# Kernel optimization log

Measured on AMD Instinct MI355X. Metric: run time of the kernel, lower is better.

The kernel has to match this reference:

```python
import jax, jax.numpy as jnp
import numpy as np

B, N, D, H = 2, 2048, 128, 128  # batch, n_nodes, node_dim, hidden_dim
HQ = H // 4
EPS_DIST = 1e-8
EPS_LN = 1e-5


def setup_inputs() -> dict:
    key = jax.random.key(0)
    ks = jax.random.split(key, 12)
    s = 0.02
    return {
        "h": jax.random.normal(ks[0], (B, N, D), jnp.float32),
        "coords": jax.random.uniform(ks[1], (B, N, 2), jnp.float32),
        "Wq": jax.random.normal(ks[2], (D, H), jnp.float32) * s,
        "bq": jnp.zeros((H,), jnp.float32),
        "Wk": jax.random.normal(ks[3], (D, H), jnp.float32) * s,
        "bk": jnp.zeros((H,), jnp.float32),
        "Wv": jax.random.normal(ks[4], (D, H), jnp.float32) * s,
        "bv": jnp.zeros((H,), jnp.float32),
        "Wd1": jax.random.normal(ks[5], (1, HQ), jnp.float32) * s,
        "bd1": jnp.zeros((HQ,), jnp.float32),
        "Wd2": jax.random.normal(ks[6], (HQ, 1), jnp.float32) * s,
        "bd2": jnp.zeros((1,), jnp.float32),
        "Wo": jax.random.normal(ks[7], (H, D), jnp.float32) * s,
        "bo": jnp.zeros((D,), jnp.float32),
        "gamma": jnp.ones((D,), jnp.float32),
        "beta": jnp.zeros((D,), jnp.float32),
    }


def reference(h, coords, Wq, bq, Wk, bk, Wv, bv, Wd1, bd1, Wd2, bd2, Wo, bo, gamma, beta):
    q = h @ Wq + bq                      # (B, N, H)
    k = h @ Wk + bk
    v = h @ Wv + bv
    scores = jnp.einsum('bnh,bmh->bnm', q, k) / jnp.sqrt(jnp.float32(H))  # (B,N,N)
    # pairwise Euclidean distances
    diff = coords[:, :, None, :] - coords[:, None, :, :]                  # (B,N,N,2)
    dist = jnp.sqrt(jnp.sum(diff * diff, axis=-1, keepdims=True) + EPS_DIST)  # (B,N,N,1)
    hmid = jax.nn.silu(dist @ Wd1 + bd1)                                  # (B,N,N,HQ)
    dist_bias = (hmid @ Wd2 + bd2)[..., 0]                                # (B,N,N)
    attn = jax.nn.softmax(scores + dist_bias, axis=-1)
    out = jnp.einsum('bnm,bmh->bnh', attn, v)                             # (B,N,H)
    out = jax.nn.silu(out @ Wo + bo)                                      # (B,N,D)
    res = h + out
    mu = jnp.mean(res, axis=-1, keepdims=True)
    var = jnp.mean((res - mu) ** 2, axis=-1, keepdims=True)
    return (res - mu) / jnp.sqrt(var + EPS_LN) * gamma + beta
```

## Files before the change

### kernel.cpp

```cpp
#include <hip/hip_runtime.h>
#include <hip/hip_bf16.h>

#define B_ 2
#define N_ 2048
#define D_ 128
#define H_ 128
#define HQ_ 32
#define ROWS_ (B_*N_)
#define KS_ 16
#define KPP_ (N_/KS_)
#define DMAX_ 1.4143f
#define SCALE_ 0.08838834764831845f

typedef __bf16 bf16x8 __attribute__((ext_vector_type(8)));
typedef float  f32x4  __attribute__((ext_vector_type(4)));
typedef unsigned short ushort8 __attribute__((ext_vector_type(8)));

#define Q_OFF    0
#define K_OFF    (ROWS_*H_*2)
#define V_OFF    (2*ROWS_*H_*2)
#define L_OFF    (3*ROWS_*H_*2)
#define OP_OFF   (L_OFF + ROWS_*KS_*4)

__global__ __launch_bounds__(384) void qkv_kernel(
    const float* __restrict__ h,
    const float* __restrict__ Wq, const float* __restrict__ bq,
    const float* __restrict__ Wk, const float* __restrict__ bk,
    const float* __restrict__ Wv, const float* __restrict__ bv,
    __bf16* __restrict__ qb, __bf16* __restrict__ kb, __bf16* __restrict__ vb)
{
    __shared__ __align__(16) float hs[8][128];
    const int t = threadIdx.x;
    const int row0 = blockIdx.x * 8;
    for (int idx = t; idx < 1024; idx += 384) hs[idx >> 7][idx & 127] = h[row0 * 128 + idx];
    __syncthreads();

    const int which = t >> 7;
    const int c = t & 127;
    const float* W    = which == 0 ? Wq : (which == 1 ? Wk : Wv);
    const float* bias = which == 0 ? bq : (which == 1 ? bk : bv);
    __bf16* outp      = which == 0 ? qb : (which == 1 ? kb : vb);
    const float scale = which == 0 ? SCALE_ : 1.f;

    float acc[8];
    #pragma unroll
    for (int r = 0; r < 8; ++r) acc[r] = 0.f;

    #pragma unroll 8
    for (int d = 0; d < 128; ++d) {
        float w = W[d * 128 + c];
        #pragma unroll
        for (int r = 0; r < 8; ++r) acc[r] = fmaf(hs[r][d], w, acc[r]);
    }
    const float bvv = bias[c];
    #pragma unroll
    for (int r = 0; r < 8; ++r)
        outp[(size_t)(row0 + r) * 128 + c] = (__bf16)((acc[r] + bvv) * scale);
}

__global__ __launch_bounds__(256, 4) void attn_kernel(
    const __bf16* __restrict__ qb, const __bf16* __restrict__ kb, const __bf16* __restrict__ vb,
    const float* __restrict__ coords,
    const float* __restrict__ Wd1, const float* __restrict__ bd1,
    const float* __restrict__ Wd2, const float* __restrict__ bd2,
    __bf16* __restrict__ Opb, float* __restrict__ Larr)
{
    __shared__ __align__(16) unsigned int Vsu[2][128][20];
    __shared__ __align__(16) __bf16 Pl[4][16][40];

    const int t    = threadIdx.x;
    const int wid  = t >> 6;
    const int lane = t & 63;
    const int l16  = lane & 15;
    const int g    = lane >> 4;
    const int qbase = blockIdx.x * 64 + wid * 16;
    const int p     = blockIdx.y;
    const int b     = qbase >> 11;

    float c0, c1, c2, c3, c4;
    {
        const int j = lane & 31;
        const float w1 = Wd1[j], b1 = bd1[j];
        const float w2h = Wd2[j] * 0.5f;
        float gv[5];
        #pragma unroll
        for (int i = 0; i < 5; ++i) {
            float d = (DMAX_ * 0.25f) * (float)i;
            float x = fmaf(d, w1, b1);
            gv[i] = (x / (1.f + __expf(-x))) * w2h;
        }
        #pragma unroll
        for (int i = 0; i < 5; ++i)
            #pragma unroll
            for (int off = 1; off < 64; off <<= 1) gv[i] += __shfl_xor(gv[i], off);
        const float bd2v = bd2[0];
        float g0 = gv[0] + bd2v, g1 = gv[1] + bd2v, g2 = gv[2] + bd2v,
              g3 = gv[3] + bd2v, g4 = gv[4] + bd2v;
        c0 = g0;
        c1 = -2.0833333333f*g0 + 4.f*g1 - 3.f*g2 + 1.3333333333f*g3 - 0.25f*g4;
        c2 =  1.4583333333f*g0 - 4.3333333333f*g1 + 4.75f*g2 - 2.3333333333f*g3 + 0.4583333333f*g4;
        c3 = -0.4166666667f*g0 + 1.5f*g1 - 2.f*g2 + 1.1666666667f*g3 - 0.25f*g4;
        c4 =  0.0416666667f*g0 - 0.1666666667f*g1 + 0.25f*g2 - 0.1666666667f*g3 + 0.0416666667f*g4;
    }

    bf16x8 qf[4];
    const __bf16* qrow = qb + (size_t)(qbase + l16) * H_;
    #pragma unroll
    for (int kk = 0; kk < 4; ++kk) qf[kk] = *(const bf16x8*)(qrow + kk * 32 + g * 8);

    float cx[4], cy[4];
    #pragma unroll
    for (int i = 0; i < 4; ++i) {
        int qr = qbase + g * 4 + i;
        cx[i] = coords[qr * 2]; cy[i] = coords[qr * 2 + 1];
    }

    float l_i[4] = {0.f, 0.f, 0.f, 0.f};
    f32x4 O[8];
    #pragma unroll
    for (int c = 0; c < 8; ++c) O[c] = (f32x4){0.f, 0.f, 0.f, 0.f};

    const int kp = t & 15, co = t >> 4;
    const int kgbase = (b << 11) + p * KPP_;
    const int NT = KPP_ / 32;

    {
        const __bf16* sp = vb + (size_t)(kgbase + 2 * kp) * H_ + co * 8;
        bf16x8 va = *(const bf16x8*)sp;
        bf16x8 vb2 = *(const bf16x8*)(sp + H_);
        ushort8 ua = __builtin_bit_cast(ushort8, va);
        ushort8 ub = __builtin_bit_cast(ushort8, vb2);
        #pragma unroll
        for (int j = 0; j < 8; ++j)
            Vsu[0][co * 8 + j][kp] = (unsigned)ua[j] | ((unsigned)ub[j] << 16);
    }

    for (int kt = 0; kt < NT; ++kt) {
        __syncthreads();

        bf16x8 nva, nvb;
        if (kt + 1 < NT) {
            const __bf16* sp = vb + (size_t)(kgbase + (kt + 1) * 32 + 2 * kp) * H_ + co * 8;
            nva = *(const bf16x8*)sp;
            nvb = *(const bf16x8*)(sp + H_);
        }

        const int kg = kgbase + kt * 32;
        #pragma unroll
        for (int mt = 0; mt < 2; ++mt) {
            f32x4 acc = (f32x4){0.f, 0.f, 0.f, 0.f};
            const __bf16* krow = kb + (size_t)(kg + mt * 16 + l16) * H_;
            #pragma unroll
            for (int kk = 0; kk < 4; ++kk) {
                bf16x8 kf = *(const bf16x8*)(krow + kk * 32 + g * 8);
                acc = __builtin_amdgcn_mfma_f32_16x16x32_bf16(qf[kk], kf, acc, 0, 0, 0);
            }
            float2 kc = *(const float2*)&coords[(kg + mt * 16 + l16) * 2];
            #pragma unroll
            for (int i = 0; i < 4; ++i) {
                float dx = cx[i] - kc.x, dy = cy[i] - kc.y;
                float dist = sqrtf(fmaf(dx, dx, fmaf(dy, dy, 1e-8f)));
                float s4 = dist * (4.0f / DMAX_);
                float bias = fmaf(fmaf(fmaf(fmaf(c4, s4, c3), s4, c2), s4, c1), s4, c0);
                float sc = fminf(acc[i] + bias, 60.f);
                float pe = __expf(sc);
                l_i[i] += pe;
                Pl[wid][g * 4 + i][mt * 16 + l16] = (__bf16)pe;
            }
        }

        if (kt + 1 < NT) {
            ushort8 ua = __builtin_bit_cast(ushort8, nva);
            ushort8 ub = __builtin_bit_cast(ushort8, nvb);
            #pragma unroll
            for (int j = 0; j < 8; ++j)
                Vsu[(kt + 1) & 1][co * 8 + j][kp] = (unsigned)ua[j] | ((unsigned)ub[j] << 16);
        }

        bf16x8 pf = *(const bf16x8*)&Pl[wid][l16][g * 8];
        #pragma unroll
        for (int c = 0; c < 8; ++c) {
            bf16x8 vf = *(const bf16x8*)&Vsu[kt & 1][c * 16 + l16][g * 4];
            O[c] = __builtin_amdgcn_mfma_f32_16x16x32_bf16(pf, vf, O[c], 0, 0, 0);
        }
    }

    #pragma unroll
    for (int c = 0; c < 8; ++c)
        #pragma unroll
        for (int i = 0; i < 4; ++i)
            Opb[((size_t)p * ROWS_ + qbase + g * 4 + i) * H_ + c * 16 + l16] = (__bf16)O[c][i];

    #pragma unroll
    for (int i = 0; i < 4; ++i) {
        float lv = l_i[i];
        lv += __shfl_xor(lv, 1); lv += __shfl_xor(lv, 2);
        lv += __shfl_xor(lv, 4); lv += __shfl_xor(lv, 8);
        if (l16 == 0) Larr[(qbase + g * 4 + i) * KS_ + p] = lv;
    }
}

__global__ __launch_bounds__(128) void final_kernel(
    const __bf16* __restrict__ Opb, const float* __restrict__ Larr,
    const float* __restrict__ h, const float* __restrict__ Wo, const float* __restrict__ bo,
    const float* __restrict__ gamma, const float* __restrict__ beta, float* __restrict__ out)
{
    __shared__ __align__(16) float as_[4][128];
    __shared__ float redS[2][4], redQ[2][4];
    const int t = threadIdx.x;
    const int row0 = blockIdx.x * 4;

    #pragma unroll
    for (int r = 0; r < 4; ++r) {
        int row = row0 + r;
        float acc = 0.f, lsum = 0.f;
        #pragma unroll
        for (int p = 0; p < KS_; ++p) {
            acc  += (float)Opb[((size_t)p * ROWS_ + row) * H_ + t];
            lsum += Larr[row * KS_ + p];
        }
        as_[r][t] = acc / lsum;
    }
    __syncthreads();

    float acc4[4] = {0.f, 0.f, 0.f, 0.f};
    #pragma unroll 4
    for (int d4 = 0; d4 < 32; ++d4) {
        float w0 = Wo[(d4 * 4 + 0) * 128 + t];
        float w1 = Wo[(d4 * 4 + 1) * 128 + t];
        float w2 = Wo[(d4 * 4 + 2) * 128 + t];
        float w3 = Wo[(d4 * 4 + 3) * 128 + t];
        #pragma unroll
        for (int r = 0; r < 4; ++r) {
            f32x4 a_ = *(const f32x4*)&as_[r][d4 * 4];
            acc4[r] = fmaf(a_[0], w0, acc4[r]);
            acc4[r] = fmaf(a_[1], w1, acc4[r]);
            acc4[r] = fmaf(a_[2], w2, acc4[r]);
            acc4[r] = fmaf(a_[3], w3, acc4[r]);
        }
    }

    const float bov = bo[t], gv = gamma[t], bvv = beta[t];
    const int wh = t >> 6;
    float res[4];
    #pragma unroll
    for (int r = 0; r < 4; ++r) {
        float x = acc4[r] + bov;
        float sl = x / (1.f + __expf(-x));
        res[r] = h[(size_t)(row0 + r) * 128 + t] + sl;
    }

    #pragma unroll
    for (int r = 0; r < 4; ++r) {
        float s1 = res[r], s2 = res[r] * res[r];
        #pragma unroll
        for (int off = 32; off >= 1; off >>= 1) {
            s1 += __shfl_xor(s1, off);
            s2 += __shfl_xor(s2, off);
        }
        if ((t & 63) == 0) { redS[wh][r] = s1; redQ[wh][r] = s2; }
    }
    __syncthreads();
    #pragma unroll
    for (int r = 0; r < 4; ++r) {
        float sum = redS[0][r] + redS[1][r];
        float sq  = redQ[0][r] + redQ[1][r];
        float mu  = sum * (1.f / 128.f);
        float var = sq * (1.f / 128.f) - mu * mu;
        out[(size_t)(row0 + r) * 128 + t] = (res[r] - mu) * rsqrtf(var + 1e-5f) * gv + bvv;
    }
}

extern "C" void kernel_launch(void* const* d_in, const int* in_sizes, int n_in,
                              void* d_out, int out_size, void* d_ws, size_t ws_size,
                              hipStream_t stream)
{
    const float* h      = (const float*)d_in[0];
    const float* coords = (const float*)d_in[1];
    const float* Wq = (const float*)d_in[2];  const float* bq = (const float*)d_in[3];
    const float* Wk = (const float*)d_in[4];  const float* bk = (const float*)d_in[5];
    const float* Wv = (const float*)d_in[6];  const float* bv = (const float*)d_in[7];
    const float* Wd1 = (const float*)d_in[8]; const float* bd1 = (const float*)d_in[9];
    const float* Wd2 = (const float*)d_in[10];const float* bd2 = (const float*)d_in[11];
    const float* Wo = (const float*)d_in[12]; const float* bo = (const float*)d_in[13];
    const float* gamma = (const float*)d_in[14]; const float* beta = (const float*)d_in[15];

    char* ws = (char*)d_ws;
    __bf16* qb = (__bf16*)(ws + Q_OFF);
    __bf16* kb = (__bf16*)(ws + K_OFF);
    __bf16* vb = (__bf16*)(ws + V_OFF);
    float* Larr  = (float*)(ws + L_OFF);
    __bf16* Opb  = (__bf16*)(ws + OP_OFF);

    qkv_kernel<<<ROWS_ / 8, 384, 0, stream>>>(h, Wq, bq, Wk, bk, Wv, bv, qb, kb, vb);
    attn_kernel<<<dim3(ROWS_ / 64, KS_), 256, 0, stream>>>(qb, kb, vb, coords,
                                                           Wd1, bd1, Wd2, bd2, Opb, Larr);
    final_kernel<<<ROWS_ / 4, 128, 0, stream>>>(Opb, Larr, h, Wo, bo, gamma, beta, (float*)d_out);
}
```

Measured before the change: 59.12 us.

## Use exp2 with folded log2e, pack partial outputs, enlarge qkv and final tiles

```diff
diff --git a/kernel.cpp b/kernel.cpp
--- a/kernel.cpp
+++ b/kernel.cpp
@@ -11,10 +11,22 @@
 #define KPP_ (N_/KS_)
 #define DMAX_ 1.4143f
 #define SCALE_ 0.08838834764831845f
+#define LOG2E_ 1.4426950408889634f
 
 typedef __bf16 bf16x8 __attribute__((ext_vector_type(8)));
 typedef float  f32x4  __attribute__((ext_vector_type(4)));
 typedef unsigned short ushort8 __attribute__((ext_vector_type(8)));
+
+#if __has_builtin(__builtin_amdgcn_exp2f)
+#define EXP2F_ __builtin_amdgcn_exp2f
+#else
+#define EXP2F_ exp2f
+#endif
+#if __has_builtin(__builtin_amdgcn_sqrtf)
+#define SQRTF_ __builtin_amdgcn_sqrtf
+#else
+#define SQRTF_ sqrtf
+#endif
 
 #define Q_OFF    0
 #define K_OFF    (ROWS_*H_*2)
@@ -29,10 +41,10 @@
     const float* __restrict__ Wv, const float* __restrict__ bv,
     __bf16* __restrict__ qb, __bf16* __restrict__ kb, __bf16* __restrict__ vb)
 {
-    __shared__ __align__(16) float hs[8][128];
+    __shared__ __align__(16) float hs[16][128];
     const int t = threadIdx.x;
-    const int row0 = blockIdx.x * 8;
-    for (int idx = t; idx < 1024; idx += 384) hs[idx >> 7][idx & 127] = h[row0 * 128 + idx];
+    const int row0 = blockIdx.x * 16;
+    for (int idx = t; idx < 2048; idx += 384) hs[idx >> 7][idx & 127] = h[row0 * 128 + idx];
     __syncthreads();
 
     const int which = t >> 7;
@@ -40,21 +52,21 @@
     const float* W    = which == 0 ? Wq : (which == 1 ? Wk : Wv);
     const float* bias = which == 0 ? bq : (which == 1 ? bk : bv);
     __bf16* outp      = which == 0 ? qb : (which == 1 ? kb : vb);
-    const float scale = which == 0 ? SCALE_ : 1.f;
-
-    float acc[8];
-    #pragma unroll
-    for (int r = 0; r < 8; ++r) acc[r] = 0.f;
+    const float scale = which == 0 ? (SCALE_ * LOG2E_) : 1.f;
+
+    float acc[16];
+    #pragma unroll
+    for (int r = 0; r < 16; ++r) acc[r] = 0.f;
 
     #pragma unroll 8
     for (int d = 0; d < 128; ++d) {
         float w = W[d * 128 + c];
         #pragma unroll
-        for (int r = 0; r < 8; ++r) acc[r] = fmaf(hs[r][d], w, acc[r]);
+        for (int r = 0; r < 16; ++r) acc[r] = fmaf(hs[r][d], w, acc[r]);
     }
     const float bvv = bias[c];
     #pragma unroll
-    for (int r = 0; r < 8; ++r)
+    for (int r = 0; r < 16; ++r)
         outp[(size_t)(row0 + r) * 128 + c] = (__bf16)((acc[r] + bvv) * scale);
 }
 
@@ -63,7 +75,7 @@
     const float* __restrict__ coords,
     const float* __restrict__ Wd1, const float* __restrict__ bd1,
     const float* __restrict__ Wd2, const float* __restrict__ bd2,
-    __bf16* __restrict__ Opb, float* __restrict__ Larr)
+    unsigned int* __restrict__ Opb32, float* __restrict__ Larr)
 {
     __shared__ __align__(16) unsigned int Vsu[2][128][20];
     __shared__ __align__(16) __bf16 Pl[4][16][40];
@@ -94,8 +106,9 @@
             #pragma unroll
             for (int off = 1; off < 64; off <<= 1) gv[i] += __shfl_xor(gv[i], off);
         const float bd2v = bd2[0];
-        float g0 = gv[0] + bd2v, g1 = gv[1] + bd2v, g2 = gv[2] + bd2v,
-              g3 = gv[3] + bd2v, g4 = gv[4] + bd2v;
+        float g0 = (gv[0] + bd2v) * LOG2E_, g1 = (gv[1] + bd2v) * LOG2E_,
+              g2 = (gv[2] + bd2v) * LOG2E_, g3 = (gv[3] + bd2v) * LOG2E_,
+              g4 = (gv[4] + bd2v) * LOG2E_;
         c0 = g0;
         c1 = -2.0833333333f*g0 + 4.f*g1 - 3.f*g2 + 1.3333333333f*g3 - 0.25f*g4;
         c2 =  1.4583333333f*g0 - 4.3333333333f*g1 + 4.75f*g2 - 2.3333333333f*g3 + 0.4583333333f*g4;
@@ -159,11 +172,11 @@
             #pragma unroll
             for (int i = 0; i < 4; ++i) {
                 float dx = cx[i] - kc.x, dy = cy[i] - kc.y;
-                float dist = sqrtf(fmaf(dx, dx, fmaf(dy, dy, 1e-8f)));
+                float dist = SQRTF_(fmaf(dx, dx, fmaf(dy, dy, 1e-8f)));
                 float s4 = dist * (4.0f / DMAX_);
                 float bias = fmaf(fmaf(fmaf(fmaf(c4, s4, c3), s4, c2), s4, c1), s4, c0);
-                float sc = fminf(acc[i] + bias, 60.f);
-                float pe = __expf(sc);
+                float sc = fminf(acc[i] + bias, 80.f);
+                float pe = EXP2F_(sc);
                 l_i[i] += pe;
                 Pl[wid][g * 4 + i][mt * 16 + l16] = (__bf16)pe;
             }
@@ -185,11 +198,15 @@
         }
     }
 
+    const size_t rpbase = (size_t)p * (ROWS_ / 2) + (qbase >> 1) + g * 2;
     #pragma unroll
     for (int c = 0; c < 8; ++c)
         #pragma unroll
-        for (int i = 0; i < 4; ++i)
-            Opb[((size_t)p * ROWS_ + qbase + g * 4 + i) * H_ + c * 16 + l16] = (__bf16)O[c][i];
+        for (int ip = 0; ip < 2; ++ip) {
+            unsigned lo = __builtin_bit_cast(unsigned, O[c][2 * ip]);
+            unsigned hi = __builtin_bit_cast(unsigned, O[c][2 * ip + 1]);
+            Opb32[(rpbase + ip) * H_ + c * 16 + l16] = (hi & 0xffff0000u) | (lo >> 16);
+        }
 
     #pragma unroll
     for (int i = 0; i < 4; ++i) {
@@ -200,39 +217,53 @@
     }
 }
 
-__global__ __launch_bounds__(128) void final_kernel(
-    const __bf16* __restrict__ Opb, const float* __restrict__ Larr,
+__global__ __launch_bounds__(256) void final_kernel(
+    const unsigned int* __restrict__ Opb32, const float* __restrict__ Larr,
     const float* __restrict__ h, const float* __restrict__ Wo, const float* __restrict__ bo,
     const float* __restrict__ gamma, const float* __restrict__ beta, float* __restrict__ out)
 {
-    __shared__ __align__(16) float as_[4][128];
-    __shared__ float redS[2][4], redQ[2][4];
+    __shared__ __align__(16) float as_[8][128];
+    __shared__ float redS[4][4], redQ[4][4];
     const int t = threadIdx.x;
-    const int row0 = blockIdx.x * 4;
-
-    #pragma unroll
-    for (int r = 0; r < 4; ++r) {
-        int row = row0 + r;
-        float acc = 0.f, lsum = 0.f;
+    const int c = t & 127;
+    const int rh = t >> 7;
+    const int bx = blockIdx.x;
+    const int row0 = (bx & 63) * 64 + (bx >> 6) * 8;
+
+    #pragma unroll
+    for (int pr = 0; pr < 2; ++pr) {
+        int r0 = rh * 4 + pr * 2;
+        int row = row0 + r0;
+        size_t rp = (size_t)row >> 1;
+        float accL = 0.f, accH = 0.f, lsumL = 0.f, lsumH = 0.f;
         #pragma unroll
         for (int p = 0; p < KS_; ++p) {
-            acc  += (float)Opb[((size_t)p * ROWS_ + row) * H_ + t];
-            lsum += Larr[row * KS_ + p];
-        }
-        as_[r][t] = acc / lsum;
+            unsigned v = Opb32[((size_t)p * (ROWS_ / 2) + rp) * H_ + c];
+            accL += __uint_as_float(v << 16);
+            accH += __uint_as_float(v & 0xffff0000u);
+        }
+        #pragma unroll
+        for (int q4 = 0; q4 < 4; ++q4) {
+            f32x4 lL = *(const f32x4*)&Larr[row * KS_ + q4 * 4];
+            f32x4 lH = *(const f32x4*)&Larr[(row + 1) * KS_ + q4 * 4];
+            lsumL += lL[0] + lL[1] + lL[2] + lL[3];
+            lsumH += lH[0] + lH[1] + lH[2] + lH[3];
+        }
+        as_[r0][c]     = accL / lsumL;
+        as_[r0 + 1][c] = accH / lsumH;
     }
     __syncthreads();
 
     float acc4[4] = {0.f, 0.f, 0.f, 0.f};
     #pragma unroll 4
     for (int d4 = 0; d4 < 32; ++d4) {
-        float w0 = Wo[(d4 * 4 + 0) * 128 + t];
-        float w1 = Wo[(d4 * 4 + 1) * 128 + t];
-        float w2 = Wo[(d4 * 4 + 2) * 128 + t];
-        float w3 = Wo[(d4 * 4 + 3) * 128 + t];
+        float w0 = Wo[(d4 * 4 + 0) * 128 + c];
+        float w1 = Wo[(d4 * 4 + 1) * 128 + c];
+        float w2 = Wo[(d4 * 4 + 2) * 128 + c];
+        float w3 = Wo[(d4 * 4 + 3) * 128 + c];
         #pragma unroll
         for (int r = 0; r < 4; ++r) {
-            f32x4 a_ = *(const f32x4*)&as_[r][d4 * 4];
+            f32x4 a_ = *(const f32x4*)&as_[rh * 4 + r][d4 * 4];
             acc4[r] = fmaf(a_[0], w0, acc4[r]);
             acc4[r] = fmaf(a_[1], w1, acc4[r]);
             acc4[r] = fmaf(a_[2], w2, acc4[r]);
@@ -240,14 +271,14 @@
         }
     }
 
-    const float bov = bo[t], gv = gamma[t], bvv = beta[t];
-    const int wh = t >> 6;
+    const float bov = bo[c], gv = gamma[c], bvv = beta[c];
+    const int wv = t >> 6;
     float res[4];
     #pragma unroll
     for (int r = 0; r < 4; ++r) {
         float x = acc4[r] + bov;
         float sl = x / (1.f + __expf(-x));
-        res[r] = h[(size_t)(row0 + r) * 128 + t] + sl;
+        res[r] = h[(size_t)(row0 + rh * 4 + r) * 128 + c] + sl;
     }
 
     #pragma unroll
@@ -258,16 +289,16 @@
             s1 += __shfl_xor(s1, off);
             s2 += __shfl_xor(s2, off);
         }
-        if ((t & 63) == 0) { redS[wh][r] = s1; redQ[wh][r] = s2; }
+        if ((t & 63) == 0) { redS[wv][r] = s1; redQ[wv][r] = s2; }
     }
     __syncthreads();
     #pragma unroll
     for (int r = 0; r < 4; ++r) {
-        float sum = redS[0][r] + redS[1][r];
-        float sq  = redQ[0][r] + redQ[1][r];
+        float sum = redS[2 * rh][r] + redS[2 * rh + 1][r];
+        float sq  = redQ[2 * rh][r] + redQ[2 * rh + 1][r];
         float mu  = sum * (1.f / 128.f);
         float var = sq * (1.f / 128.f) - mu * mu;
-        out[(size_t)(row0 + r) * 128 + t] = (res[r] - mu) * rsqrtf(var + 1e-5f) * gv + bvv;
+        out[(size_t)(row0 + rh * 4 + r) * 128 + c] = (res[r] - mu) * rsqrtf(var + 1e-5f) * gv + bvv;
     }
 }
 
@@ -289,11 +320,11 @@
     __bf16* qb = (__bf16*)(ws + Q_OFF);
     __bf16* kb = (__bf16*)(ws + K_OFF);
     __bf16* vb = (__bf16*)(ws + V_OFF);
-    float* Larr  = (float*)(ws + L_OFF);
-    __bf16* Opb  = (__bf16*)(ws + OP_OFF);
-
-    qkv_kernel<<<ROWS_ / 8, 384, 0, stream>>>(h, Wq, bq, Wk, bk, Wv, bv, qb, kb, vb);
+    float* Larr        = (float*)(ws + L_OFF);
+    unsigned int* Opb32 = (unsigned int*)(ws + OP_OFF);
+
+    qkv_kernel<<<ROWS_ / 16, 384, 0, stream>>>(h, Wq, bq, Wk, bk, Wv, bv, qb, kb, vb);
     attn_kernel<<<dim3(ROWS_ / 64, KS_), 256, 0, stream>>>(qb, kb, vb, coords,
-                                                           Wd1, bd1, Wd2, bd2, Opb, Larr);
-    final_kernel<<<ROWS_ / 4, 128, 0, stream>>>(Opb, Larr, h, Wo, bo, gamma, beta, (float*)d_out);
+                                                           Wd1, bd1, Wd2, bd2, Opb32, Larr);
+    final_kernel<<<ROWS_ / 8, 256, 0, stream>>>(Opb32, Larr, h, Wo, bo, gamma, beta, (float*)d_out);
 }
```

New measurement: 74.87 us. +26.6%, slower.
